# Kernel tuning notes

Measured on AMD Instinct MI355X. Metric: run time of the kernel, lower is better.

The kernel has to match this reference:

```python
import jax, jax.numpy as jnp
import numpy as np

B, S, D, H = 4, 4096, 1024, 1024


def log_g(x):
    # where(x >= 0, log(relu(x) + 0.5), -softplus(-x)); relu(x)+0.5 >= 0.5 so log is safe
    return jnp.where(x >= 0, jnp.log(jax.nn.relu(x) + 0.5), -jax.nn.softplus(-x))


def setup_inputs() -> dict:
    key = jax.random.key(0)
    ks = jax.random.split(key, 8)
    scale = 1.0 / np.sqrt(D)
    return {
        "x_t": jax.random.normal(ks[0], (B, S, D), dtype=jnp.float32),
        "pre_h": jax.random.normal(ks[1], (B, 1, H), dtype=jnp.float32),
        "W_f": jax.random.uniform(ks[2], (H, D), jnp.float32, -scale, scale),
        "b_f": jax.random.uniform(ks[3], (H,), jnp.float32, -scale, scale),
        "W_i": jax.random.uniform(ks[4], (H, D), jnp.float32, -scale, scale),
        "b_i": jax.random.uniform(ks[5], (H,), jnp.float32, -scale, scale),
        "W_h": jax.random.uniform(ks[6], (H, D), jnp.float32, -scale, scale),
        "b_h": jax.random.uniform(ks[7], (H,), jnp.float32, -scale, scale),
    }


def reference(x_t, pre_h, W_f, b_f, W_i, b_i, W_h, b_h):
    sp = jax.nn.softplus
    f_pre = jnp.einsum("bsd,hd->bsh", x_t, W_f) + b_f
    i_pre = jnp.einsum("bsd,hd->bsh", x_t, W_i) + b_i
    h_pre = jnp.einsum("bsd,hd->bsh", x_t, W_h) + b_h

    diff = sp(-f_pre) - sp(-i_pre)
    log_f = -sp(diff)        # (B, S, H)
    log_i = -sp(-diff)       # (B, S, H)

    log_h0 = log_g(pre_h)                 # (B, 1, H)
    log_tilde_h = log_g(h_pre)            # (B, S, H)
    log_values = jnp.concatenate([log_h0, log_i + log_tilde_h], axis=1)  # (B, S+1, H)

    # parallel_scan_log: pad cumsum at END of seq dim (as in source: F.pad(..., (0,0,0,1)))
    a_star = jnp.pad(jnp.cumsum(log_f, axis=1), ((0, 0), (0, 1), (0, 0)))  # (B, S+1, H)
    log_h0_plus_b_star = jax.lax.cumlogsumexp(log_values - a_star, axis=1)
    log_h = a_star + log_h0_plus_b_star
    return jnp.exp(log_h)[:, 1:]  # (B, S, H)
```

## Files before the change

kernel.cpp:

```cpp
#include <hip/hip_runtime.h>
#include <hip/hip_bf16.h>
#include <math.h>

#define B_DIM 4
#define S_DIM 4096
#define K_DIM 1024
#define H_DIM 1024
#define M_DIM (B_DIM * S_DIM)

#define BMT 128
#define BNT 64
#define KT_ITERS (K_DIM / 32)

#define NCHUNK 64
#define CLEN (S_DIM / NCHUNK)

typedef __attribute__((ext_vector_type(8))) _Float16 f16x8;
typedef __attribute__((ext_vector_type(4))) _Float16 f16x4;
typedef __attribute__((ext_vector_type(4))) float f32x4;

__device__ __forceinline__ float sp_f(float x) {
    return fmaxf(x, 0.0f) + __logf(1.0f + __expf(-fabsf(x)));
}
__device__ __forceinline__ float log_g_f(float x) {
    return (x >= 0.0f) ? __logf(x + 0.5f) : -sp_f(-x);
}
__device__ __forceinline__ float logaddexp_f(float a, float b) {
    float m = fmaxf(a, b);
    return m + __logf(1.0f + __expf(-fabsf(a - b)));
}
__device__ __forceinline__ float exp_sat(float x) {
    return __expf(fminf(x, 85.0f));
}

__device__ __forceinline__ void gl_lds16(const void* g, void* l) {
    __builtin_amdgcn_global_load_lds(
        (const __attribute__((address_space(1))) unsigned int*)g,
        (__attribute__((address_space(3))) unsigned int*)l, 16, 0, 0);
}

__global__ __launch_bounds__(256) void conv_f16(
    const float* __restrict__ src, _Float16* __restrict__ dst, int n4)
{
    int i = blockIdx.x * 256 + threadIdx.x;
    if (i >= n4) return;
    float4 v = ((const float4*)src)[i];
    f16x4 o = {(_Float16)v.x, (_Float16)v.y, (_Float16)v.z, (_Float16)v.w};
    ((f16x4*)dst)[i] = o;
}

__global__ __launch_bounds__(256, 3) void gemm3(
    const _Float16* __restrict__ xh,
    const _Float16* __restrict__ wh,
    const float* __restrict__ bfp, const float* __restrict__ bip,
    const float* __restrict__ bhp,
    float* __restrict__ lf_out, __hip_bfloat16* __restrict__ w_out)
{
    __shared__ __align__(16) char smem[20480];

    const int tid = threadIdx.x;
    const int lane = tid & 63;
    const int wv = tid >> 6;
    const int wm = wv >> 1;
    const int wn = wv & 1;

    int flat = blockIdx.y * 128 + blockIdx.x;
    int st = flat >> 7, w7 = flat & 127;
    int mt = ((st >> 1) << 4) + (w7 & 15);
    int nt = ((st & 1) << 3) + (w7 >> 4);
    const int row0 = mt * BMT;
    const int col0 = nt * BNT;

    const int arow = tid & 127, akq = tid >> 7;
    size_t ga0 = ((size_t)(row0 + arow) * K_DIM + (akq + 0) * 8) * 2;
    size_t ga1 = ga0 + 32;
    const int brow = tid & 63, bkq = tid >> 6;
    size_t gb0 = ((size_t)(0 * H_DIM + col0 + brow) * K_DIM + bkq * 8) * 2;
    size_t gb1 = ((size_t)(1 * H_DIM + col0 + brow) * K_DIM + bkq * 8) * 2;
    size_t gb2 = ((size_t)(2 * H_DIM + col0 + brow) * K_DIM + bkq * 8) * 2;

    const char* px = (const char*)xh;
    const char* pw = (const char*)wh;

    int aoff[4], boff[2];
#pragma unroll
    for (int mi = 0; mi < 4; ++mi)
        aoff[mi] = ((lane >> 4) << 11) + ((wm * 64 + mi * 16 + (lane & 15)) << 4);
#pragma unroll
    for (int nj = 0; nj < 2; ++nj)
        boff[nj] = ((lane >> 4) << 10) + ((wn * 32 + nj * 16 + (lane & 15)) << 4);

    f32x4 acc[3][4][2];
#pragma unroll
    for (int g = 0; g < 3; ++g)
#pragma unroll
        for (int mi = 0; mi < 4; ++mi)
#pragma unroll
            for (int nj = 0; nj < 2; ++nj)
                acc[g][mi][nj] = (f32x4){0.f, 0.f, 0.f, 0.f};

    for (int kt = 0; kt < KT_ITERS; ++kt) {
        __syncthreads();
        gl_lds16(px + ga0, smem + tid * 16);
        gl_lds16(px + ga1, smem + 4096 + tid * 16);
        gl_lds16(pw + gb0, smem + 8192 + tid * 16);
        gl_lds16(pw + gb1, smem + 12288 + tid * 16);
        gl_lds16(pw + gb2, smem + 16384 + tid * 16);
        ga0 += 64; ga1 += 64; gb0 += 64; gb1 += 64; gb2 += 64;
        __syncthreads();

        f16x8 a[4];
#pragma unroll
        for (int mi = 0; mi < 4; ++mi)
            a[mi] = *(const f16x8*)(smem + aoff[mi]);
#pragma unroll
        for (int g = 0; g < 3; ++g) {
            const char* bb = smem + 8192 + g * 4096;
            f16x8 b0 = *(const f16x8*)(bb + boff[0]);
            f16x8 b1 = *(const f16x8*)(bb + boff[1]);
#pragma unroll
            for (int mi = 0; mi < 4; ++mi) {
                acc[g][mi][0] = __builtin_amdgcn_mfma_f32_16x16x32_f16(a[mi], b0, acc[g][mi][0], 0, 0, 0);
                acc[g][mi][1] = __builtin_amdgcn_mfma_f32_16x16x32_f16(a[mi], b1, acc[g][mi][1], 0, 0, 0);
            }
        }
    }

    int nidx[2];
    float bfv[2], biv[2], bhv[2];
#pragma unroll
    for (int nj = 0; nj < 2; ++nj) {
        nidx[nj] = col0 + wn * 32 + nj * 16 + (lane & 15);
        bfv[nj] = bfp[nidx[nj]];
        biv[nj] = bip[nidx[nj]];
        bhv[nj] = bhp[nidx[nj]];
    }
#pragma unroll
    for (int mi = 0; mi < 4; ++mi) {
#pragma unroll
        for (int r = 0; r < 4; ++r) {
            int m = row0 + wm * 64 + mi * 16 + ((lane >> 4) << 2) + r;
#pragma unroll
            for (int nj = 0; nj < 2; ++nj) {
                float f_pre = acc[0][mi][nj][r] + bfv[nj];
                float i_pre = acc[1][mi][nj][r] + biv[nj];
                float h_pre = acc[2][mi][nj][r] + bhv[nj];
                float diff = sp_f(-f_pre) - sp_f(-i_pre);
                float lfv = -sp_f(diff);
                float wv_ = -sp_f(-diff) + log_g_f(h_pre);
                size_t o = (size_t)m * H_DIM + nidx[nj];
                lf_out[o] = lfv;
                w_out[o] = __float2bfloat16(wv_);
            }
        }
    }
}

__global__ __launch_bounds__(256) void scan_pass_a(
    const float* __restrict__ lf, const __hip_bfloat16* __restrict__ w,
    float2* __restrict__ agg)
{
    int tid = blockIdx.x * blockDim.x + threadIdx.x;
    int h = tid & (H_DIM - 1);
    int b = (tid >> 10) & (B_DIM - 1);
    int q = tid >> 12;

    int tstart = q * CLEN + 1;
    int tend = (q == NCHUNK - 1) ? (S_DIM - 1) : (q * CLEN + CLEN);

    size_t idx = (size_t)(b * S_DIM + tstart) * H_DIM + h;
    float c = 0.0f, r = -INFINITY;
    for (int t = tstart; t <= tend; ++t) {
        c += lf[idx];
        r = logaddexp_f(r, __bfloat162float(w[idx - H_DIM]) - c);
        idx += H_DIM;
    }
    agg[(size_t)(b * H_DIM + h) * NCHUNK + q] = make_float2(c, r);
}

__global__ __launch_bounds__(256) void scan_pass_b(
    const float* __restrict__ lf, const float* __restrict__ preh,
    const float2* __restrict__ agg, float2* __restrict__ prefix)
{
    int col = blockIdx.x * blockDim.x + threadIdx.x;
    int h = col & (H_DIM - 1);
    int b = col >> 10;

    float lf0 = lf[(size_t)(b * S_DIM) * H_DIM + h];
    float C = lf0;
    float R = log_g_f(preh[b * H_DIM + h]) - lf0;
    for (int q = 0; q < NCHUNK; ++q) {
        prefix[(size_t)col * NCHUNK + q] = make_float2(C, R);
        float2 a = agg[(size_t)col * NCHUNK + q];
        float Rn = logaddexp_f(R, a.y - C);
        C += a.x;
        R = Rn;
    }
}

__global__ __launch_bounds__(256) void scan_pass_c(
    const float* __restrict__ lf, const __hip_bfloat16* __restrict__ w,
    const float2* __restrict__ prefix, float* __restrict__ out)
{
    int tid = blockIdx.x * blockDim.x + threadIdx.x;
    int h = tid & (H_DIM - 1);
    int b = (tid >> 10) & (B_DIM - 1);
    int q = tid >> 12;

    float2 p = prefix[(size_t)(b * H_DIM + h) * NCHUNK + q];
    float C = p.x, R = p.y;

    int tstart = q * CLEN + 1;
    int tend = (q == NCHUNK - 1) ? (S_DIM - 1) : (q * CLEN + CLEN);

    size_t idx = (size_t)(b * S_DIM + tstart) * H_DIM + h;
    for (int t = tstart; t <= tend; ++t) {
        C += lf[idx];
        R = logaddexp_f(R, __bfloat162float(w[idx - H_DIM]) - C);
        out[idx - H_DIM] = exp_sat(C + R);
        idx += H_DIM;
    }
    if (q == NCHUNK - 1) {
        R = logaddexp_f(R, __bfloat162float(w[idx - H_DIM]));
        out[idx - H_DIM] = exp_sat(R);
    }
}

extern "C" void kernel_launch(void* const* d_in, const int* in_sizes, int n_in,
                              void* d_out, int out_size, void* d_ws, size_t ws_size,
                              hipStream_t stream) {
    const float* x    = (const float*)d_in[0];
    const float* preh = (const float*)d_in[1];
    const float* Wf   = (const float*)d_in[2];
    const float* bf   = (const float*)d_in[3];
    const float* Wi   = (const float*)d_in[4];
    const float* bi   = (const float*)d_in[5];
    const float* Wh   = (const float*)d_in[6];
    const float* bh   = (const float*)d_in[7];
    float* out = (float*)d_out;

    _Float16* xh = (_Float16*)d_ws;
    _Float16* wh = xh + (size_t)M_DIM * K_DIM;
    float* lf = (float*)(wh + (size_t)3 * H_DIM * K_DIM);
    __hip_bfloat16* wbuf = (__hip_bfloat16*)(lf + (size_t)M_DIM * H_DIM);
    float2* agg = (float2*)(wbuf + (size_t)M_DIM * H_DIM);
    float2* prefix = agg + (size_t)B_DIM * H_DIM * NCHUNK;

    conv_f16<<<(M_DIM * K_DIM / 4) / 256, 256, 0, stream>>>(x, xh, M_DIM * K_DIM / 4);
    conv_f16<<<(H_DIM * K_DIM / 4) / 256, 256, 0, stream>>>(Wf, wh, H_DIM * K_DIM / 4);
    conv_f16<<<(H_DIM * K_DIM / 4) / 256, 256, 0, stream>>>(
        Wi, wh + (size_t)H_DIM * K_DIM, H_DIM * K_DIM / 4);
    conv_f16<<<(H_DIM * K_DIM / 4) / 256, 256, 0, stream>>>(
        Wh, wh + (size_t)2 * H_DIM * K_DIM, H_DIM * K_DIM / 4);

    gemm3<<<dim3(M_DIM / BMT, H_DIM / BNT), 256, 0, stream>>>(
        xh, wh, bf, bi, bh, lf, wbuf);

    scan_pass_a<<<(B_DIM * H_DIM * NCHUNK) / 256, 256, 0, stream>>>(lf, wbuf, agg);
    scan_pass_b<<<(B_DIM * H_DIM) / 256, 256, 0, stream>>>(lf, preh, agg, prefix);
    scan_pass_c<<<(B_DIM * H_DIM * NCHUNK) / 256, 256, 0, stream>>>(lf, wbuf, prefix, out);
}
```

Measured before the change: 394.9 us.

## Store log_f and w intermediates in fp16 and simplify GEMM tile mapping

The GEMM epilogue now writes log_f as fp16 instead of fp32 and the w term as fp16 instead of bf16. This halves the lf intermediate traffic read by the two scan passes. The swizzled block-to-tile mapping is replaced with a plain grid where x indexes N tiles and y indexes M tiles, and global offsets become 32-bit unsigned. Storing log_f in fp16 loses precision in a cumulative sum over 4096 steps, which risks accuracy drift, and dropping the swizzle may change L2 reuse.

```diff
diff --git a/kernel.cpp b/kernel.cpp
--- a/kernel.cpp
+++ b/kernel.cpp
@@ -54,7 +54,7 @@
     const _Float16* __restrict__ wh,
     const float* __restrict__ bfp, const float* __restrict__ bip,
     const float* __restrict__ bhp,
-    float* __restrict__ lf_out, __hip_bfloat16* __restrict__ w_out)
+    _Float16* __restrict__ lf_out, _Float16* __restrict__ w_out)
 {
     __shared__ __align__(16) char smem[20480];
 
@@ -64,23 +64,18 @@
     const int wm = wv >> 1;
     const int wn = wv & 1;
 
-    int flat = blockIdx.y * 128 + blockIdx.x;
-    int st = flat >> 7, w7 = flat & 127;
-    int mt = ((st >> 1) << 4) + (w7 & 15);
-    int nt = ((st & 1) << 3) + (w7 >> 4);
-    const int row0 = mt * BMT;
-    const int col0 = nt * BNT;
+    const int row0 = blockIdx.y * BMT;
+    const int col0 = blockIdx.x * BNT;
 
     const int arow = tid & 127, akq = tid >> 7;
-    size_t ga0 = ((size_t)(row0 + arow) * K_DIM + (akq + 0) * 8) * 2;
-    size_t ga1 = ga0 + 32;
+    unsigned ga0 = (unsigned)(((row0 + arow) * K_DIM + akq * 8) * 2);
     const int brow = tid & 63, bkq = tid >> 6;
-    size_t gb0 = ((size_t)(0 * H_DIM + col0 + brow) * K_DIM + bkq * 8) * 2;
-    size_t gb1 = ((size_t)(1 * H_DIM + col0 + brow) * K_DIM + bkq * 8) * 2;
-    size_t gb2 = ((size_t)(2 * H_DIM + col0 + brow) * K_DIM + bkq * 8) * 2;
-
-    const char* px = (const char*)xh;
-    const char* pw = (const char*)wh;
+    unsigned gb0 = (unsigned)(((0 * H_DIM + col0 + brow) * K_DIM + bkq * 8) * 2);
+    unsigned gb1 = (unsigned)(((1 * H_DIM + col0 + brow) * K_DIM + bkq * 8) * 2);
+    unsigned gb2 = (unsigned)(((2 * H_DIM + col0 + brow) * K_DIM + bkq * 8) * 2);
+
+    const char* __restrict__ px = (const char*)xh;
+    const char* __restrict__ pw = (const char*)wh;
 
     int aoff[4], boff[2];
 #pragma unroll
@@ -102,11 +97,11 @@
     for (int kt = 0; kt < KT_ITERS; ++kt) {
         __syncthreads();
         gl_lds16(px + ga0, smem + tid * 16);
-        gl_lds16(px + ga1, smem + 4096 + tid * 16);
+        gl_lds16(px + ga0 + 32, smem + 4096 + tid * 16);
         gl_lds16(pw + gb0, smem + 8192 + tid * 16);
         gl_lds16(pw + gb1, smem + 12288 + tid * 16);
         gl_lds16(pw + gb2, smem + 16384 + tid * 16);
-        ga0 += 64; ga1 += 64; gb0 += 64; gb1 += 64; gb2 += 64;
+        ga0 += 64; gb0 += 64; gb1 += 64; gb2 += 64;
         __syncthreads();
 
         f16x8 a[4];
@@ -149,15 +144,15 @@
                 float lfv = -sp_f(diff);
                 float wv_ = -sp_f(-diff) + log_g_f(h_pre);
                 size_t o = (size_t)m * H_DIM + nidx[nj];
-                lf_out[o] = lfv;
-                w_out[o] = __float2bfloat16(wv_);
+                lf_out[o] = (_Float16)lfv;
+                w_out[o] = (_Float16)wv_;
             }
         }
     }
 }
 
 __global__ __launch_bounds__(256) void scan_pass_a(
-    const float* __restrict__ lf, const __hip_bfloat16* __restrict__ w,
+    const _Float16* __restrict__ lf, const _Float16* __restrict__ w,
     float2* __restrict__ agg)
 {
     int tid = blockIdx.x * blockDim.x + threadIdx.x;
@@ -171,22 +166,22 @@
     size_t idx = (size_t)(b * S_DIM + tstart) * H_DIM + h;
     float c = 0.0f, r = -INFINITY;
     for (int t = tstart; t <= tend; ++t) {
-        c += lf[idx];
-        r = logaddexp_f(r, __bfloat162float(w[idx - H_DIM]) - c);
+        c += (float)lf[idx];
+        r = logaddexp_f(r, (float)w[idx - H_DIM] - c);
         idx += H_DIM;
     }
     agg[(size_t)(b * H_DIM + h) * NCHUNK + q] = make_float2(c, r);
 }
 
 __global__ __launch_bounds__(256) void scan_pass_b(
-    const float* __restrict__ lf, const float* __restrict__ preh,
+    const _Float16* __restrict__ lf, const float* __restrict__ preh,
     const float2* __restrict__ agg, float2* __restrict__ prefix)
 {
     int col = blockIdx.x * blockDim.x + threadIdx.x;
     int h = col & (H_DIM - 1);
     int b = col >> 10;
 
-    float lf0 = lf[(size_t)(b * S_DIM) * H_DIM + h];
+    float lf0 = (float)lf[(size_t)(b * S_DIM) * H_DIM + h];
     float C = lf0;
     float R = log_g_f(preh[b * H_DIM + h]) - lf0;
     for (int q = 0; q < NCHUNK; ++q) {
@@ -199,7 +194,7 @@
 }
 
 __global__ __launch_bounds__(256) void scan_pass_c(
-    const float* __restrict__ lf, const __hip_bfloat16* __restrict__ w,
+    const _Float16* __restrict__ lf, const _Float16* __restrict__ w,
     const float2* __restrict__ prefix, float* __restrict__ out)
 {
     int tid = blockIdx.x * blockDim.x + threadIdx.x;
@@ -215,13 +210,13 @@
 
     size_t idx = (size_t)(b * S_DIM + tstart) * H_DIM + h;
     for (int t = tstart; t <= tend; ++t) {
-        C += lf[idx];
-        R = logaddexp_f(R, __bfloat162float(w[idx - H_DIM]) - C);
+        C += (float)lf[idx];
+        R = logaddexp_f(R, (float)w[idx - H_DIM] - C);
         out[idx - H_DIM] = exp_sat(C + R);
         idx += H_DIM;
     }
     if (q == NCHUNK - 1) {
-        R = logaddexp_f(R, __bfloat162float(w[idx - H_DIM]));
+        R = logaddexp_f(R, (float)w[idx - H_DIM]);
         out[idx - H_DIM] = exp_sat(R);
     }
 }
@@ -241,8 +236,8 @@
 
     _Float16* xh = (_Float16*)d_ws;
     _Float16* wh = xh + (size_t)M_DIM * K_DIM;
-    float* lf = (float*)(wh + (size_t)3 * H_DIM * K_DIM);
-    __hip_bfloat16* wbuf = (__hip_bfloat16*)(lf + (size_t)M_DIM * H_DIM);
+    _Float16* lf = wh + (size_t)3 * H_DIM * K_DIM;
+    _Float16* wbuf = lf + (size_t)M_DIM * H_DIM;
     float2* agg = (float2*)(wbuf + (size_t)M_DIM * H_DIM);
     float2* prefix = agg + (size_t)B_DIM * H_DIM * NCHUNK;
 
@@ -253,7 +248,7 @@
     conv_f16<<<(H_DIM * K_DIM / 4) / 256, 256, 0, stream>>>(
         Wh, wh + (size_t)2 * H_DIM * K_DIM, H_DIM * K_DIM / 4);
 
-    gemm3<<<dim3(M_DIM / BMT, H_DIM / BNT), 256, 0, stream>>>(
+    gemm3<<<dim3(H_DIM / BNT, M_DIM / BMT), 256, 0, stream>>>(
         xh, wh, bf, bi, bh, lf, wbuf);
 
     scan_pass_a<<<(B_DIM * H_DIM * NCHUNK) / 256, 256, 0, stream>>>(lf, wbuf, agg);
```

After: 393.0 us. About the same (-0.5%).
